# Kernel tuning notes

Hardware: AMD Instinct MI355X
Metric: run time of the kernel (lower is better)

The kernel has to match this reference:

```python
import jax, jax.numpy as jnp
import numpy as np

# dims: M=MC samples, B=graphs, K=latent, H=decoder hidden, N=max nodes, P=permutations
M, B, K, H, N, F_DIM, P = 4, 256, 64, 1024, 50, 3, 64
E = N * (N - 1) // 2  # reduced adjacency = strictly lower triangle
COEFF_A = 1.0
BETA = 1.0
TRIL_I, TRIL_J = np.tril_indices(N, -1)


def setup_inputs() -> dict:
    key = jax.random.key(0)
    ks = jax.random.split(key, 12)
    mean = 0.5 * jax.random.normal(ks[0], (B, K), dtype=jnp.float32)
    logvar = 0.1 * jax.random.normal(ks[1], (B, K), dtype=jnp.float32)
    eps = jax.random.normal(ks[2], (M, B, K), dtype=jnp.float32)
    W1 = jax.random.normal(ks[3], (K, H), dtype=jnp.float32) / np.sqrt(K)
    b1 = jnp.zeros((H,), jnp.float32)
    WA = jax.random.normal(ks[4], (H, E), dtype=jnp.float32) / np.sqrt(H)
    bA = jnp.zeros((E,), jnp.float32)
    WF = jax.random.normal(ks[5], (H, N * F_DIM), dtype=jnp.float32) / np.sqrt(H)
    bF = jnp.zeros((N * F_DIM,), jnp.float32)
    # symmetric binary adjacency with zero diagonal
    U = jax.random.bernoulli(ks[6], 0.15, (B, N, N)).astype(jnp.float32)
    Au = jnp.triu(U, 1)
    A_in = Au + jnp.swapaxes(Au, -1, -2)
    # two bernoulli attributes + one one-hot-categorical attribute (over nodes)
    fb = jax.random.bernoulli(ks[7], 0.3, (B, N, 2)).astype(jnp.float32)
    idx = jax.random.randint(ks[8], (B,), 0, N)
    oh = jax.nn.one_hot(idx, N, dtype=jnp.float32)  # (B, N)
    Fx = jnp.concatenate([fb, oh[..., None]], axis=-1)  # (B, N, 3)
    coeff_Fx = jnp.ones((F_DIM,), jnp.float32)
    permutations = jax.vmap(lambda k: jax.random.permutation(k, N))(
        jax.random.split(ks[9], P)).astype(jnp.int32)  # (P, N)
    return dict(mean=mean, logvar=logvar, eps=eps, W1=W1, b1=b1, WA=WA, bA=bA,
                WF=WF, bF=bF, A_in=A_in, Fx=Fx, coeff_Fx=coeff_Fx,
                permutations=permutations)


def _bernoulli_logprob(x, logits):
    # sum of elementwise Bernoulli log-prob over last axis
    return jnp.sum(x * jax.nn.log_sigmoid(logits)
                   + (1.0 - x) * jax.nn.log_sigmoid(-logits), axis=-1)


def reference(mean, logvar, eps, W1, b1, WA, bA, WF, bF, A_in, Fx, coeff_Fx,
              permutations):
    # pathwise (reparametrised) latent samples: (M, B, K)
    Z = mean + jnp.exp(0.5 * logvar) * eps
    # MLP decoder
    h = jax.nn.relu(Z @ W1 + b1)                       # (M, B, H)
    logits_A = h @ WA + bA                              # (M, B, E)
    logits_Fx = (h @ WF + bF).reshape(M, B, N, F_DIM)   # (M, B, N, F)
    # permutation-matched adjacency: A_perm[b,p,i,j] = A_in[b, perm[p,i], perm[p,j]]
    A_perm = A_in[:, permutations[:, :, None], permutations[:, None, :]]  # (B,P,N,N)
    A_red = A_perm[..., TRIL_I, TRIL_J].reshape(B * P, E)                 # (B*P, E)
    lA = jnp.repeat(logits_A, P, axis=1)                                  # (M, B*P, E)
    nce_A = _bernoulli_logprob(A_red, lA).mean(axis=0)                    # (B*P,)
    nce_A = nce_A.reshape(B, P).max(axis=1)                               # (B,)
    # attribute log-probs: two bernoulli (sum over nodes), one categorical over nodes
    lp_bern = jnp.sum(
        Fx[..., :2] * jax.nn.log_sigmoid(logits_Fx[..., :2])
        + (1.0 - Fx[..., :2]) * jax.nn.log_sigmoid(-logits_Fx[..., :2]),
        axis=-2)                                                          # (M, B, 2)
    lp_cat = jnp.sum(Fx[..., 2] * jax.nn.log_softmax(logits_Fx[..., 2], axis=-1),
                     axis=-1)                                             # (M, B)
    nce_Fx = jnp.concatenate([lp_bern.mean(0), lp_cat.mean(0)[:, None]], axis=-1)  # (B, F)
    # KL(q(z|x) || N(0, I))
    kld = 0.5 * jnp.sum(jnp.exp(logvar) + mean ** 2 - 1.0 - logvar, axis=-1)  # (B,)
    return COEFF_A * nce_A + nce_Fx @ coeff_Fx - BETA * kld
```

## Files before the change

### kernel.cpp

```cpp
#include <hip/hip_runtime.h>
#include <math.h>

#define MM 4
#define BB 256
#define KK 64
#define HH 1024
#define NN 50
#define EE 1225
#define PP 64
#define CTOT 1375
#define NPAD 1408

typedef short short8 __attribute__((ext_vector_type(8)));
typedef float floatx4 __attribute__((ext_vector_type(4)));
typedef unsigned short ushort;

__device__ __forceinline__ ushort f2bf(float f) {
    union { float f; unsigned u; } v; v.f = f;
    unsigned r = v.u + 0x7fffu + ((v.u >> 16) & 1u);
    return (ushort)(r >> 16);
}

__device__ __forceinline__ float logsigm(float l) {
    return -(fmaxf(l, 0.0f) + log1pf(expf(-fabsf(l))));
}

__device__ __forceinline__ float wsum64(float v) {
    #pragma unroll
    for (int m = 1; m < 64; m <<= 1) v += __shfl_xor(v, m);
    return v;
}
__device__ __forceinline__ float wmax64(float v) {
    #pragma unroll
    for (int m = 1; m < 64; m <<= 1) v = fmaxf(v, __shfl_xor(v, m));
    return v;
}

__global__ __launch_bounds__(256) void kA(const float* __restrict__ mean,
                                          const float* __restrict__ logvar,
                                          const float* __restrict__ eps,
                                          const float* __restrict__ W1,
                                          const float* __restrict__ b1,
                                          const float* __restrict__ WA,
                                          const float* __restrict__ WF,
                                          const float* __restrict__ A,
                                          ushort* __restrict__ hB,
                                          ushort* __restrict__ Wt,
                                          float* __restrict__ Sneg,
                                          int*   __restrict__ edgesG,
                                          int*   __restrict__ cntG,
                                          float* __restrict__ kldG) {
    const int t = threadIdx.x;
    __shared__ float smem[64 * 65];
    __shared__ int cnt;

    if (blockIdx.x < 256) {
        const int b = blockIdx.x;
        float4* z4 = (float4*)smem;
        if (t == 0) cnt = 0;
        if (t < 64) {
            float mv = mean[b * 64 + t];
            float lv = logvar[b * 64 + t];
            float sd = expf(0.5f * lv);
            float4 z;
            z.x = mv + sd * eps[(0 * BB + b) * 64 + t];
            z.y = mv + sd * eps[(1 * BB + b) * 64 + t];
            z.z = mv + sd * eps[(2 * BB + b) * 64 + t];
            z.w = mv + sd * eps[(3 * BB + b) * 64 + t];
            z4[t] = z;
            float term = 0.5f * (expf(lv) + mv * mv - 1.0f - lv);
            term = wsum64(term);
            if (t == 0) kldG[b] = term;
        }
        if (t < 4) Sneg[b * 4 + t] = 0.0f;
        __syncthreads();
        const int j0 = t * 4;
        float acc[4][4] = {};
        #pragma unroll 8
        for (int k = 0; k < 64; k++) {
            float4 w = *(const float4*)&W1[k * HH + j0];
            float4 z = z4[k];
            acc[0][0] += z.x * w.x; acc[0][1] += z.x * w.y; acc[0][2] += z.x * w.z; acc[0][3] += z.x * w.w;
            acc[1][0] += z.y * w.x; acc[1][1] += z.y * w.y; acc[1][2] += z.y * w.z; acc[1][3] += z.y * w.w;
            acc[2][0] += z.z * w.x; acc[2][1] += z.z * w.y; acc[2][2] += z.z * w.z; acc[2][3] += z.z * w.w;
            acc[3][0] += z.w * w.x; acc[3][1] += z.w * w.y; acc[3][2] += z.w * w.z; acc[3][3] += z.w * w.w;
        }
        float4 bb = *(const float4*)&b1[j0];
        #pragma unroll
        for (int m = 0; m < 4; m++) {
            unsigned u0 = ((unsigned)f2bf(fmaxf(acc[m][0] + bb.x, 0.f))) |
                          ((unsigned)f2bf(fmaxf(acc[m][1] + bb.y, 0.f)) << 16);
            unsigned u1 = ((unsigned)f2bf(fmaxf(acc[m][2] + bb.z, 0.f))) |
                          ((unsigned)f2bf(fmaxf(acc[m][3] + bb.w, 0.f)) << 16);
            uint2 u; u.x = u0; u.y = u1;
            *(uint2*)&hB[(b * 4 + m) * HH + j0] = u;
        }
        for (int x = t; x < 2500; x += 256) {
            int i = x / NN, j = x - i * NN;
            if (j < i) {
                float a = A[b * 2500 + x];
                if (a != 0.0f) { int id = atomicAdd(&cnt, 1); edgesG[b * 256 + id] = (i << 8) | j; }
            }
        }
        __syncthreads();
        if (t == 0) cntG[b] = cnt;
    } else {
        const int id = blockIdx.x - 256;
        const int kt = id & 15, nt = id >> 4;
        float* T = smem;
        const int k0 = kt * 64, n0 = nt * 64;
        #pragma unroll
        for (int i = 0; i < 16; i++) {
            int x = i * 256 + t;
            int kk = x >> 6, nn = x & 63;
            int gn = n0 + nn, gk = k0 + kk;
            float v = 0.f;
            if (gn < EE)        v = WA[gk * EE + gn];
            else if (gn < CTOT) v = WF[gk * 150 + (gn - EE)];
            T[kk * 65 + nn] = v;
        }
        __syncthreads();
        #pragma unroll
        for (int i = 0; i < 16; i++) {
            int x = i * 256 + t;
            int nn = x >> 6, kk = x & 63;
            Wt[(n0 + nn) * 1024 + k0 + kk] = f2bf(T[kk * 65 + nn]);
        }
    }
}

__global__ __launch_bounds__(256) void k2(const ushort* __restrict__ hB,
                                          const ushort* __restrict__ Wt,
                                          const float* __restrict__ bA,
                                          const float* __restrict__ bF,
                                          float* __restrict__ Lbar,
                                          float* __restrict__ Sneg,
                                          float* __restrict__ lgF) {
    const int ct = blockIdx.x;
    const int rt = blockIdx.y;
    const int t = threadIdx.x;
    const int w = t >> 6, lane = t & 63;
    const int wm = w >> 1, wn = w & 1;
    const int quad = lane >> 4, l16 = lane & 15;
    __shared__ short As[64][72];
    __shared__ short Bs[128][72];
    floatx4 acc[2][4] = {};
    const int row0 = rt * 64, col0 = ct * 128;

    const int rA0 = t >> 3, koA = (t & 7) * 8;
    const int rA1 = (256 + t) >> 3;
    const int rB0 = t >> 3;
    const ushort* pA0 = hB + (row0 + rA0) * 1024 + koA;
    const ushort* pA1 = hB + (row0 + rA1) * 1024 + koA;
    const ushort* pB  = Wt + (col0 + rB0) * 1024 + koA;

    short8 ra[2], rb[4];
    ra[0] = *(const short8*)(pA0);
    ra[1] = *(const short8*)(pA1);
    #pragma unroll
    for (int i = 0; i < 4; i++) rb[i] = *(const short8*)(pB + i * 32 * 1024);

    for (int ch = 0; ch < 16; ch++) {
        __syncthreads();
        *(short8*)&As[rA0][koA] = ra[0];
        *(short8*)&As[rA1][koA] = ra[1];
        #pragma unroll
        for (int i = 0; i < 4; i++) *(short8*)&Bs[i * 32 + rB0][koA] = rb[i];
        __syncthreads();
        if (ch < 15) {
            const int off = (ch + 1) * 64;
            ra[0] = *(const short8*)(pA0 + off);
            ra[1] = *(const short8*)(pA1 + off);
            #pragma unroll
            for (int i = 0; i < 4; i++) rb[i] = *(const short8*)(pB + i * 32 * 1024 + off);
        }
        #pragma unroll
        for (int kk = 0; kk < 2; kk++) {
            int ko = kk * 32 + quad * 8;
            short8 a0 = *(const short8*)&As[wm * 32 + l16][ko];
            short8 a1 = *(const short8*)&As[wm * 32 + 16 + l16][ko];
            short8 b0 = *(const short8*)&Bs[wn * 64 + l16][ko];
            short8 b1 = *(const short8*)&Bs[wn * 64 + 16 + l16][ko];
            short8 b2 = *(const short8*)&Bs[wn * 64 + 32 + l16][ko];
            short8 b3 = *(const short8*)&Bs[wn * 64 + 48 + l16][ko];
            acc[0][0] = __builtin_amdgcn_mfma_f32_16x16x32_bf16(a0, b0, acc[0][0], 0, 0, 0);
            acc[0][1] = __builtin_amdgcn_mfma_f32_16x16x32_bf16(a0, b1, acc[0][1], 0, 0, 0);
            acc[0][2] = __builtin_amdgcn_mfma_f32_16x16x32_bf16(a0, b2, acc[0][2], 0, 0, 0);
            acc[0][3] = __builtin_amdgcn_mfma_f32_16x16x32_bf16(a0, b3, acc[0][3], 0, 0, 0);
            acc[1][0] = __builtin_amdgcn_mfma_f32_16x16x32_bf16(a1, b0, acc[1][0], 0, 0, 0);
            acc[1][1] = __builtin_amdgcn_mfma_f32_16x16x32_bf16(a1, b1, acc[1][1], 0, 0, 0);
            acc[1][2] = __builtin_amdgcn_mfma_f32_16x16x32_bf16(a1, b2, acc[1][2], 0, 0, 0);
            acc[1][3] = __builtin_amdgcn_mfma_f32_16x16x32_bf16(a1, b3, acc[1][3], 0, 0, 0);
        }
    }

    #pragma unroll
    for (int mi = 0; mi < 2; mi++) {
        const int grow = row0 + wm * 32 + mi * 16 + quad * 4;
        const int b = grow >> 2;
        float sn0 = 0.f, sn1 = 0.f, sn2 = 0.f, sn3 = 0.f;
        #pragma unroll
        for (int ni = 0; ni < 4; ni++) {
            int gc = col0 + wn * 64 + ni * 16 + l16;
            floatx4 a = acc[mi][ni];
            if (gc < EE) {
                float bias = bA[gc];
                float l0 = a[0] + bias, l1 = a[1] + bias, l2 = a[2] + bias, l3 = a[3] + bias;
                Lbar[b * EE + gc] = 0.25f * (l0 + l1 + l2 + l3);
                sn0 += logsigm(l0); sn1 += logsigm(l1); sn2 += logsigm(l2); sn3 += logsigm(l3);
            } else if (gc < CTOT) {
                int c2 = gc - EE;
                float bias = bF[c2];
                lgF[(b * 4 + 0) * 150 + c2] = a[0] + bias;
                lgF[(b * 4 + 1) * 150 + c2] = a[1] + bias;
                lgF[(b * 4 + 2) * 150 + c2] = a[2] + bias;
                lgF[(b * 4 + 3) * 150 + c2] = a[3] + bias;
            }
        }
        #pragma unroll
        for (int msk = 1; msk < 16; msk <<= 1) {
            sn0 += __shfl_xor(sn0, msk);
            sn1 += __shfl_xor(sn1, msk);
            sn2 += __shfl_xor(sn2, msk);
            sn3 += __shfl_xor(sn3, msk);
        }
        if (l16 == 0) {
            atomicAdd(&Sneg[b * 4 + 0], sn0);
            atomicAdd(&Sneg[b * 4 + 1], sn1);
            atomicAdd(&Sneg[b * 4 + 2], sn2);
            atomicAdd(&Sneg[b * 4 + 3], sn3);
        }
    }
}

__global__ __launch_bounds__(256) void k4(const float* __restrict__ Fx,
                                          const float* __restrict__ coeff,
                                          const int* __restrict__ perms,
                                          const float* __restrict__ Lbar,
                                          const float* __restrict__ Sneg,
                                          const float* __restrict__ lgF,
                                          const int* __restrict__ edgesG,
                                          const int* __restrict__ cntG,
                                          const float* __restrict__ kldG,
                                          float* __restrict__ out) {
    const int b = blockIdx.x;
    const int t = threadIdx.x;
    const int w = t >> 6, lane = t & 63;
    __shared__ int   ip[PP * NN];
    __shared__ float Lb[EE];
    __shared__ int   edges[256];
    __shared__ float lgfs[600];
    __shared__ float mred[4], wmaxs[4];

    const int ne = cntG[b];
    for (int x = t; x < PP * NN; x += 256) {
        int p = x / NN, i = x - p * NN;
        ip[p * NN + perms[x]] = i;
    }
    for (int x = t; x < EE; x += 256) Lb[x] = Lbar[b * EE + x];
    for (int x = t; x < 600; x += 256) lgfs[x] = lgF[b * 600 + x];
    if (t < ne) edges[t] = edgesG[b * 256 + t];
    __syncthreads();

    {
        float l0 = 0.f, l1 = 0.f, l2 = -INFINITY, x0 = 0.f, x1 = 0.f, x2 = 0.f;
        bool v = lane < NN;
        if (v) {
            l0 = lgfs[w * 150 + lane * 3 + 0];
            l1 = lgfs[w * 150 + lane * 3 + 1];
            l2 = lgfs[w * 150 + lane * 3 + 2];
            x0 = Fx[b * 150 + lane * 3 + 0];
            x1 = Fx[b * 150 + lane * 3 + 1];
            x2 = Fx[b * 150 + lane * 3 + 2];
        }
        float mx = wmax64(l2);
        float es = v ? expf(l2 - mx) : 0.f;
        es = wsum64(es);
        float lse = mx + logf(es);
        float val = 0.f;
        if (v) {
            val = coeff[0] * (logsigm(l0) + x0 * l0)
                + coeff[1] * (logsigm(l1) + x1 * l1)
                + coeff[2] * (x2 * (l2 - lse));
        }
        val = wsum64(val);
        if (lane == 0) mred[w] = val;
    }
    __syncthreads();

    float lmax = -INFINITY;
    for (int p = w; p < PP; p += 4) {
        const int* ipp = &ip[p * NN];
        float acc = 0.f;
        for (int x = lane; x < ne; x += 64) {
            int ed = edges[x];
            int iu = ipp[ed >> 8], iv = ipp[ed & 255];
            int ii = max(iu, iv), jj = min(iu, iv);
            acc += Lb[ii * (ii - 1) / 2 + jj];
        }
        acc = wsum64(acc);
        lmax = fmaxf(lmax, acc);
    }
    if (lane == 0) wmaxs[w] = lmax;
    __syncthreads();
    if (t == 0) {
        float dmax = fmaxf(fmaxf(wmaxs[0], wmaxs[1]), fmaxf(wmaxs[2], wmaxs[3]));
        float sbar = 0.25f * (Sneg[b * 4 + 0] + Sneg[b * 4 + 1] + Sneg[b * 4 + 2] + Sneg[b * 4 + 3]);
        float fxv  = 0.25f * (mred[0] + mred[1] + mred[2] + mred[3]);
        out[b] = (sbar + dmax) + fxv - kldG[b];
    }
}

extern "C" void kernel_launch(void* const* d_in, const int* in_sizes, int n_in,
                              void* d_out, int out_size, void* d_ws, size_t ws_size,
                              hipStream_t stream) {
    const float* mean   = (const float*)d_in[0];
    const float* logvar = (const float*)d_in[1];
    const float* eps    = (const float*)d_in[2];
    const float* W1     = (const float*)d_in[3];
    const float* b1     = (const float*)d_in[4];
    const float* WA     = (const float*)d_in[5];
    const float* bA     = (const float*)d_in[6];
    const float* WF     = (const float*)d_in[7];
    const float* bF     = (const float*)d_in[8];
    const float* A      = (const float*)d_in[9];
    const float* Fx     = (const float*)d_in[10];
    const float* coeff  = (const float*)d_in[11];
    const int*   perms  = (const int*)d_in[12];
    float* out = (float*)d_out;

    ushort* Wt   = (ushort*)d_ws;
    ushort* hB   = Wt + NPAD * 1024;
    float*  Lbar = (float*)(hB + 1024 * 1024);
    float*  Sneg = Lbar + BB * EE;
    float*  lgF  = Sneg + 1024;
    int*    edgesG = (int*)(lgF + 1024 * 150);
    int*    cntG   = edgesG + 256 * 256;
    float*  kldG   = (float*)(cntG + 256);

    kA<<<dim3(608), dim3(256), 0, stream>>>(mean, logvar, eps, W1, b1, WA, WF, A,
                                            hB, Wt, Sneg, edgesG, cntG, kldG);
    k2<<<dim3(11, 16), dim3(256), 0, stream>>>(hB, Wt, bA, bF, Lbar, Sneg, lgF);
    k4<<<dim3(BB), dim3(256), 0, stream>>>(Fx, coeff, perms, Lbar, Sneg, lgF,
                                           edgesG, cntG, kldG, out);
}
```

Measured before the change: 136.2 us.

## Fuse GEMM and permutation-max kernels with a dynamic work queue and row-tile counters

Merges the decoder GEMM kernel and the per-graph permutation scoring kernel into one launch. Each block first runs its GEMM tile, then bumps a per-row-tile completion counter. It then pulls graph indices from a global atomic queue and spin-waits until all 11 column tiles for that graph's row tile have finished. This removes a kernel launch and lets the scoring tail overlap with GEMM stragglers, but it adds spin-wait synchronisation, reuses shared memory through a union, and uses only 176 blocks for the 256 graphs instead of 256.

```diff
diff --git a/kernel.cpp b/kernel.cpp
--- a/kernel.cpp
+++ b/kernel.cpp
@@ -49,7 +49,9 @@
                                           float* __restrict__ Sneg,
                                           int*   __restrict__ edgesG,
                                           int*   __restrict__ cntG,
-                                          float* __restrict__ kldG) {
+                                          float* __restrict__ kldG,
+                                          int*   __restrict__ doneRT,
+                                          int*   __restrict__ gq) {
     const int t = threadIdx.x;
     __shared__ float smem[64 * 65];
     __shared__ int cnt;
@@ -58,6 +60,10 @@
         const int b = blockIdx.x;
         float4* z4 = (float4*)smem;
         if (t == 0) cnt = 0;
+        if (b == 0) {
+            if (t < 16) doneRT[t] = 0;
+            if (t == 16) *gq = 0;
+        }
         if (t < 64) {
             float mv = mean[b * 64 + t];
             float lv = logvar[b * 64 + t];
@@ -129,21 +135,40 @@
     }
 }
 
-__global__ __launch_bounds__(256) void k2(const ushort* __restrict__ hB,
-                                          const ushort* __restrict__ Wt,
-                                          const float* __restrict__ bA,
-                                          const float* __restrict__ bF,
-                                          float* __restrict__ Lbar,
-                                          float* __restrict__ Sneg,
-                                          float* __restrict__ lgF) {
+struct SMg { short As[64][72]; short Bs[128][72]; };
+struct SMf {
+    int   ip[PP * NN];
+    float Lb[EE];
+    int   edges[256];
+    float lgfs[600];
+    float mred[4], wmaxs[4];
+    int   gcur;
+};
+union SMem { SMg g; SMf f; };
+
+__global__ __launch_bounds__(256) void k24(const ushort* __restrict__ hB,
+                                           const ushort* __restrict__ Wt,
+                                           const float* __restrict__ bA,
+                                           const float* __restrict__ bF,
+                                           const float* __restrict__ Fx,
+                                           const float* __restrict__ coeff,
+                                           const int*   __restrict__ perms,
+                                           float* __restrict__ Lbar,
+                                           float* __restrict__ Sneg,
+                                           float* __restrict__ lgF,
+                                           const int*   __restrict__ edgesG,
+                                           const int*   __restrict__ cntG,
+                                           const float* __restrict__ kldG,
+                                           int* __restrict__ doneRT,
+                                           int* __restrict__ gq,
+                                           float* __restrict__ out) {
     const int ct = blockIdx.x;
     const int rt = blockIdx.y;
     const int t = threadIdx.x;
     const int w = t >> 6, lane = t & 63;
     const int wm = w >> 1, wn = w & 1;
     const int quad = lane >> 4, l16 = lane & 15;
-    __shared__ short As[64][72];
-    __shared__ short Bs[128][72];
+    __shared__ SMem sm;
     floatx4 acc[2][4] = {};
     const int row0 = rt * 64, col0 = ct * 128;
 
@@ -162,10 +187,10 @@
 
     for (int ch = 0; ch < 16; ch++) {
         __syncthreads();
-        *(short8*)&As[rA0][koA] = ra[0];
-        *(short8*)&As[rA1][koA] = ra[1];
-        #pragma unroll
-        for (int i = 0; i < 4; i++) *(short8*)&Bs[i * 32 + rB0][koA] = rb[i];
+        *(short8*)&sm.g.As[rA0][koA] = ra[0];
+        *(short8*)&sm.g.As[rA1][koA] = ra[1];
+        #pragma unroll
+        for (int i = 0; i < 4; i++) *(short8*)&sm.g.Bs[i * 32 + rB0][koA] = rb[i];
         __syncthreads();
         if (ch < 15) {
             const int off = (ch + 1) * 64;
@@ -177,12 +202,12 @@
         #pragma unroll
         for (int kk = 0; kk < 2; kk++) {
             int ko = kk * 32 + quad * 8;
-            short8 a0 = *(const short8*)&As[wm * 32 + l16][ko];
-            short8 a1 = *(const short8*)&As[wm * 32 + 16 + l16][ko];
-            short8 b0 = *(const short8*)&Bs[wn * 64 + l16][ko];
-            short8 b1 = *(const short8*)&Bs[wn * 64 + 16 + l16][ko];
-            short8 b2 = *(const short8*)&Bs[wn * 64 + 32 + l16][ko];
-            short8 b3 = *(const short8*)&Bs[wn * 64 + 48 + l16][ko];
+            short8 a0 = *(const short8*)&sm.g.As[wm * 32 + l16][ko];
+            short8 a1 = *(const short8*)&sm.g.As[wm * 32 + 16 + l16][ko];
+            short8 b0 = *(const short8*)&sm.g.Bs[wn * 64 + l16][ko];
+            short8 b1 = *(const short8*)&sm.g.Bs[wn * 64 + 16 + l16][ko];
+            short8 b2 = *(const short8*)&sm.g.Bs[wn * 64 + 32 + l16][ko];
+            short8 b3 = *(const short8*)&sm.g.Bs[wn * 64 + 48 + l16][ko];
             acc[0][0] = __builtin_amdgcn_mfma_f32_16x16x32_bf16(a0, b0, acc[0][0], 0, 0, 0);
             acc[0][1] = __builtin_amdgcn_mfma_f32_16x16x32_bf16(a0, b1, acc[0][1], 0, 0, 0);
             acc[0][2] = __builtin_amdgcn_mfma_f32_16x16x32_bf16(a0, b2, acc[0][2], 0, 0, 0);
@@ -231,83 +256,82 @@
             atomicAdd(&Sneg[b * 4 + 3], sn3);
         }
     }
-}
-
-__global__ __launch_bounds__(256) void k4(const float* __restrict__ Fx,
-                                          const float* __restrict__ coeff,
-                                          const int* __restrict__ perms,
-                                          const float* __restrict__ Lbar,
-                                          const float* __restrict__ Sneg,
-                                          const float* __restrict__ lgF,
-                                          const int* __restrict__ edgesG,
-                                          const int* __restrict__ cntG,
-                                          const float* __restrict__ kldG,
-                                          float* __restrict__ out) {
-    const int b = blockIdx.x;
-    const int t = threadIdx.x;
-    const int w = t >> 6, lane = t & 63;
-    __shared__ int   ip[PP * NN];
-    __shared__ float Lb[EE];
-    __shared__ int   edges[256];
-    __shared__ float lgfs[600];
-    __shared__ float mred[4], wmaxs[4];
-
-    const int ne = cntG[b];
+
+    __syncthreads();
+    __threadfence();
+    if (t == 0) atomicAdd(&doneRT[rt], 1);
+
     for (int x = t; x < PP * NN; x += 256) {
         int p = x / NN, i = x - p * NN;
-        ip[p * NN + perms[x]] = i;
-    }
-    for (int x = t; x < EE; x += 256) Lb[x] = Lbar[b * EE + x];
-    for (int x = t; x < 600; x += 256) lgfs[x] = lgF[b * 600 + x];
-    if (t < ne) edges[t] = edgesG[b * 256 + t];
-    __syncthreads();
-
-    {
-        float l0 = 0.f, l1 = 0.f, l2 = -INFINITY, x0 = 0.f, x1 = 0.f, x2 = 0.f;
-        bool v = lane < NN;
-        if (v) {
-            l0 = lgfs[w * 150 + lane * 3 + 0];
-            l1 = lgfs[w * 150 + lane * 3 + 1];
-            l2 = lgfs[w * 150 + lane * 3 + 2];
-            x0 = Fx[b * 150 + lane * 3 + 0];
-            x1 = Fx[b * 150 + lane * 3 + 1];
-            x2 = Fx[b * 150 + lane * 3 + 2];
-        }
-        float mx = wmax64(l2);
-        float es = v ? expf(l2 - mx) : 0.f;
-        es = wsum64(es);
-        float lse = mx + logf(es);
-        float val = 0.f;
-        if (v) {
-            val = coeff[0] * (logsigm(l0) + x0 * l0)
-                + coeff[1] * (logsigm(l1) + x1 * l1)
-                + coeff[2] * (x2 * (l2 - lse));
-        }
-        val = wsum64(val);
-        if (lane == 0) mred[w] = val;
-    }
-    __syncthreads();
-
-    float lmax = -INFINITY;
-    for (int p = w; p < PP; p += 4) {
-        const int* ipp = &ip[p * NN];
-        float acc = 0.f;
-        for (int x = lane; x < ne; x += 64) {
-            int ed = edges[x];
-            int iu = ipp[ed >> 8], iv = ipp[ed & 255];
-            int ii = max(iu, iv), jj = min(iu, iv);
-            acc += Lb[ii * (ii - 1) / 2 + jj];
-        }
-        acc = wsum64(acc);
-        lmax = fmaxf(lmax, acc);
-    }
-    if (lane == 0) wmaxs[w] = lmax;
-    __syncthreads();
-    if (t == 0) {
-        float dmax = fmaxf(fmaxf(wmaxs[0], wmaxs[1]), fmaxf(wmaxs[2], wmaxs[3]));
-        float sbar = 0.25f * (Sneg[b * 4 + 0] + Sneg[b * 4 + 1] + Sneg[b * 4 + 2] + Sneg[b * 4 + 3]);
-        float fxv  = 0.25f * (mred[0] + mred[1] + mred[2] + mred[3]);
-        out[b] = (sbar + dmax) + fxv - kldG[b];
+        sm.f.ip[p * NN + perms[x]] = i;
+    }
+
+    for (;;) {
+        if (t == 0) sm.f.gcur = atomicAdd(gq, 1);
+        __syncthreads();
+        const int g = sm.f.gcur;
+        if (g >= 256) break;
+        const int rtn = g >> 4;
+        if (t == 0) {
+            while (atomicAdd(&doneRT[rtn], 0) < 11) {}
+        }
+        __syncthreads();
+        __threadfence();
+
+        const int ne = cntG[g];
+        for (int x = t; x < EE; x += 256) sm.f.Lb[x] = Lbar[g * EE + x];
+        for (int x = t; x < 600; x += 256) sm.f.lgfs[x] = lgF[g * 600 + x];
+        if (t < ne) sm.f.edges[t] = edgesG[g * 256 + t];
+        __syncthreads();
+
+        {
+            float l0 = 0.f, l1 = 0.f, l2 = -INFINITY, x0 = 0.f, x1 = 0.f, x2 = 0.f;
+            bool v = lane < NN;
+            if (v) {
+                l0 = sm.f.lgfs[w * 150 + lane * 3 + 0];
+                l1 = sm.f.lgfs[w * 150 + lane * 3 + 1];
+                l2 = sm.f.lgfs[w * 150 + lane * 3 + 2];
+                x0 = Fx[g * 150 + lane * 3 + 0];
+                x1 = Fx[g * 150 + lane * 3 + 1];
+                x2 = Fx[g * 150 + lane * 3 + 2];
+            }
+            float mx = wmax64(l2);
+            float es = v ? expf(l2 - mx) : 0.f;
+            es = wsum64(es);
+            float lse = mx + logf(es);
+            float val = 0.f;
+            if (v) {
+                val = coeff[0] * (logsigm(l0) + x0 * l0)
+                    + coeff[1] * (logsigm(l1) + x1 * l1)
+                    + coeff[2] * (x2 * (l2 - lse));
+            }
+            val = wsum64(val);
+            if (lane == 0) sm.f.mred[w] = val;
+        }
+        __syncthreads();
+
+        float lmax = -INFINITY;
+        for (int p = w; p < PP; p += 4) {
+            const int* ipp = &sm.f.ip[p * NN];
+            float acc2 = 0.f;
+            for (int x = lane; x < ne; x += 64) {
+                int ed = sm.f.edges[x];
+                int iu = ipp[ed >> 8], iv = ipp[ed & 255];
+                int ii = max(iu, iv), jj = min(iu, iv);
+                acc2 += sm.f.Lb[ii * (ii - 1) / 2 + jj];
+            }
+            acc2 = wsum64(acc2);
+            lmax = fmaxf(lmax, acc2);
+        }
+        if (lane == 0) sm.f.wmaxs[w] = lmax;
+        __syncthreads();
+        if (t == 0) {
+            float dmax = fmaxf(fmaxf(sm.f.wmaxs[0], sm.f.wmaxs[1]), fmaxf(sm.f.wmaxs[2], sm.f.wmaxs[3]));
+            float sbar = 0.25f * (Sneg[g * 4 + 0] + Sneg[g * 4 + 1] + Sneg[g * 4 + 2] + Sneg[g * 4 + 3]);
+            float fxv  = 0.25f * (sm.f.mred[0] + sm.f.mred[1] + sm.f.mred[2] + sm.f.mred[3]);
+            out[g] = (sbar + dmax) + fxv - kldG[g];
+        }
+        __syncthreads();
     }
 }
 
@@ -337,10 +361,12 @@
     int*    edgesG = (int*)(lgF + 1024 * 150);
     int*    cntG   = edgesG + 256 * 256;
     float*  kldG   = (float*)(cntG + 256);
+    int*    doneRT = (int*)(kldG + 256);
+    int*    gq     = doneRT + 16;
 
     kA<<<dim3(608), dim3(256), 0, stream>>>(mean, logvar, eps, W1, b1, WA, WF, A,
-                                            hB, Wt, Sneg, edgesG, cntG, kldG);
-    k2<<<dim3(11, 16), dim3(256), 0, stream>>>(hB, Wt, bA, bF, Lbar, Sneg, lgF);
-    k4<<<dim3(BB), dim3(256), 0, stream>>>(Fx, coeff, perms, Lbar, Sneg, lgF,
-                                           edgesG, cntG, kldG, out);
-}
+                                            hB, Wt, Sneg, edgesG, cntG, kldG, doneRT, gq);
+    k24<<<dim3(11, 16), dim3(256), 0, stream>>>(hB, Wt, bA, bF, Fx, coeff, perms,
+                                                Lbar, Sneg, lgF, edgesG, cntG, kldG,
+                                                doneRT, gq, out);
+}
```

After: 182.4 us. +34.0%, slower.
